# Kernel tuning notes

Hardware: AMD Instinct MI355X
Metric: run time of the kernel (lower is better)

The kernel has to match this reference:

```python
import jax, jax.numpy as jnp
from jax import lax
import numpy as np


def setup_inputs() -> dict:
    key = jax.random.key(0)
    k1, k2 = jax.random.split(key)
    x = jax.random.normal(k1, (16, 512, 512, 3), dtype=jnp.float32)
    # raw filter; module draws N(mean=10, scale=1) then normalizes to sum 1
    filt = jax.random.normal(k2, (9, 9, 1, 1), dtype=jnp.float32)
    return {"x": x, "filt": filt}


def _conv_same(a, f):
    # NHWC input, HWIO filter, SAME padding, stride 1
    return lax.conv_general_dilated(
        a, f, window_strides=(1, 1), padding="SAME",
        dimension_numbers=("NHWC", "HWIO", "NHWC"))


def reference(x, filt):
    # Keras: random_normal_variable(mean=10, scale=1) -> shift raw N(0,1) by 10
    f = filt + 10.0
    f = f / jnp.sum(f)                      # normalize BEFORE channel repeat
    f = jnp.tile(f, (1, 1, 3, 1))           # (9,9,3,1): sums over 3 input channels
    local_mean = _conv_same(x, f)           # (B,H,W,1), broadcasts over channels
    v = x - local_mean                      # (B,H,W,3)
    sigma = jnp.sqrt(_conv_same(v * v, f))  # (B,H,W,1)
    mean = jnp.mean(sigma, axis=(1, 2), keepdims=True)  # (B,1,1,1)
    return v / jnp.maximum(mean, sigma)
```

## Files before the change

kernel.cpp:

```cpp
#include <hip/hip_runtime.h>

#define BATCH 16
#define HH 512
#define WW 512
#define NPIX (BATCH * HH * WW)

#define RAD 4
#define OT 32
#define MT (OT + 2*RAD)
#define ST (MT + 2*RAD)

__global__ void norm_filter_kernel(const float* __restrict__ filt,
                                   float* __restrict__ f) {
    __shared__ float sh[128];
    int tid = threadIdx.x;
    float v = (tid < 81) ? (filt[tid] + 10.0f) : 0.0f;
    sh[tid] = v;
    __syncthreads();
    for (int o = 64; o > 0; o >>= 1) {
        if (tid < o) sh[tid] += sh[tid + o];
        __syncthreads();
    }
    float sum = sh[0];
    if (tid < 81) f[tid] = v / sum;
}

__global__ __launch_bounds__(256) void lcn_fused_kernel(
        const float* __restrict__ x, const float* __restrict__ f,
        float* __restrict__ m, float* __restrict__ sig,
        float* __restrict__ partial) {
    __shared__ float s48[ST][ST];
    __shared__ float q48[ST][ST];
    __shared__ float t40[MT][MT];
    __shared__ float wsum[4];

    const int tid = threadIdx.x;
    const int b = blockIdx.z;
    const int h0 = blockIdx.y * OT;
    const int w0 = blockIdx.x * OT;
    const float* xb = x + (size_t)b * HH * WW * 3;

#pragma unroll
    for (int k = 0; k < 9; k++) {
        const int i = tid + k * 256;
        const int r = i / ST, c = i - r * ST;
        const int gh = h0 - 2 * RAD + r, gw = w0 - 2 * RAD + c;
        float sv = 0.0f, qv = 0.0f;
        if (gh >= 0 && gh < HH && gw >= 0 && gw < WW) {
            const float* xp = xb + ((size_t)gh * WW + gw) * 3;
            float a0 = xp[0], a1 = xp[1], a2 = xp[2];
            sv = a0 + a1 + a2;
            qv = a0 * a0 + a1 * a1 + a2 * a2;
        }
        s48[r][c] = sv;
        q48[r][c] = qv;
    }
    __syncthreads();

    for (int item = tid; item < MT * (MT / 4); item += 256) {
        const int cg = item % (MT / 4);
        const int row = item / (MT / 4);
        const int c0 = 4 * cg;

        float acc0 = 0.f, acc1 = 0.f, acc2 = 0.f, acc3 = 0.f;
#pragma unroll
        for (int dh = 0; dh < 9; dh++) {
            const float4 va = *(const float4*)&s48[row + dh][c0];
            const float4 vb = *(const float4*)&s48[row + dh][c0 + 4];
            const float4 vc = *(const float4*)&s48[row + dh][c0 + 8];
            const float v[12] = {va.x, va.y, va.z, va.w,
                                 vb.x, vb.y, vb.z, vb.w,
                                 vc.x, vc.y, vc.z, vc.w};
#pragma unroll
            for (int j = 0; j < 9; j++) {
                const float fv = f[dh * 9 + j];
                acc0 += v[j] * fv;
                acc1 += v[j + 1] * fv;
                acc2 += v[j + 2] * fv;
                acc3 += v[j + 3] * fv;
            }
        }

        const float4 sc = *(const float4*)&s48[row + 4][c0 + 4];
        const float4 qc = *(const float4*)&q48[row + 4][c0 + 4];
        const int gh = h0 - RAD + row;
        const bool ghin = (gh >= 0 && gh < HH);
        const int gw0 = w0 - RAD + c0;
        float4 tv;
        tv.x = (ghin && gw0 + 0 >= 0 && gw0 + 0 < WW)
                   ? qc.x - 2.0f * acc0 * sc.x + 3.0f * acc0 * acc0 : 0.0f;
        tv.y = (ghin && gw0 + 1 >= 0 && gw0 + 1 < WW)
                   ? qc.y - 2.0f * acc1 * sc.y + 3.0f * acc1 * acc1 : 0.0f;
        tv.z = (ghin && gw0 + 2 >= 0 && gw0 + 2 < WW)
                   ? qc.z - 2.0f * acc2 * sc.z + 3.0f * acc2 * acc2 : 0.0f;
        tv.w = (ghin && gw0 + 3 >= 0 && gw0 + 3 < WW)
                   ? qc.w - 2.0f * acc3 * sc.w + 3.0f * acc3 * acc3 : 0.0f;
        *(float4*)&t40[row][c0] = tv;

        if (row >= RAD && row < RAD + OT && cg >= 1 && cg <= 8) {
            float4 mv4 = {acc0, acc1, acc2, acc3};
            *(float4*)&m[((size_t)b * HH + gh) * WW + (w0 + 4 * (cg - 1))] = mv4;
        }
    }
    __syncthreads();

    float psum = 0.0f;
    {
        const int cg = tid % (OT / 4);
        const int row = tid / (OT / 4);
        const int c0 = 4 * cg;

        float acc0 = 0.f, acc1 = 0.f, acc2 = 0.f, acc3 = 0.f;
#pragma unroll
        for (int dh = 0; dh < 9; dh++) {
            const float4 va = *(const float4*)&t40[row + dh][c0];
            const float4 vb = *(const float4*)&t40[row + dh][c0 + 4];
            const float4 vc = *(const float4*)&t40[row + dh][c0 + 8];
            const float v[12] = {va.x, va.y, va.z, va.w,
                                 vb.x, vb.y, vb.z, vb.w,
                                 vc.x, vc.y, vc.z, vc.w};
#pragma unroll
            for (int j = 0; j < 9; j++) {
                const float fv = f[dh * 9 + j];
                acc0 += v[j] * fv;
                acc1 += v[j + 1] * fv;
                acc2 += v[j + 2] * fv;
                acc3 += v[j + 3] * fv;
            }
        }
        float4 sg;
        sg.x = sqrtf(fmaxf(acc0, 0.0f));
        sg.y = sqrtf(fmaxf(acc1, 0.0f));
        sg.z = sqrtf(fmaxf(acc2, 0.0f));
        sg.w = sqrtf(fmaxf(acc3, 0.0f));
        *(float4*)&sig[((size_t)b * HH + (h0 + row)) * WW + (w0 + c0)] = sg;
        psum = sg.x + sg.y + sg.z + sg.w;
    }

#pragma unroll
    for (int o = 32; o > 0; o >>= 1) psum += __shfl_down(psum, o);
    if ((tid & 63) == 0) wsum[tid >> 6] = psum;
    __syncthreads();
    if (tid == 0)
        partial[b * 256 + blockIdx.y * 16 + blockIdx.x] =
            wsum[0] + wsum[1] + wsum[2] + wsum[3];
}

__global__ __launch_bounds__(256) void reduce_bsum_kernel(
        const float* __restrict__ partial, float* __restrict__ bsum) {
    __shared__ float wsum[4];
    const int b = blockIdx.x, tid = threadIdx.x;
    float v = partial[b * 256 + tid];
#pragma unroll
    for (int o = 32; o > 0; o >>= 1) v += __shfl_down(v, o);
    if ((tid & 63) == 0) wsum[tid >> 6] = v;
    __syncthreads();
    if (tid == 0) bsum[b] = wsum[0] + wsum[1] + wsum[2] + wsum[3];
}

__global__ __launch_bounds__(256) void final_kernel(
        const float* __restrict__ x, const float* __restrict__ m,
        const float* __restrict__ sig, const float* __restrict__ bsum,
        float* __restrict__ out) {
    const int i = blockIdx.x * 256 + threadIdx.x;
    const int b = i >> 16;
    const float mean = bsum[b] * (1.0f / (HH * WW));

    float4 mv = ((const float4*)m)[i];
    float4 sv = ((const float4*)sig)[i];
    const float4* xp = (const float4*)x + (size_t)i * 3;
    float4 a = xp[0], bb = xp[1], cc = xp[2];

    float r0 = __builtin_amdgcn_rcpf(fmaxf(mean, sv.x));
    float r1 = __builtin_amdgcn_rcpf(fmaxf(mean, sv.y));
    float r2 = __builtin_amdgcn_rcpf(fmaxf(mean, sv.z));
    float r3 = __builtin_amdgcn_rcpf(fmaxf(mean, sv.w));

    float4 o0, o1, o2;
    o0.x = (a.x - mv.x) * r0;
    o0.y = (a.y - mv.x) * r0;
    o0.z = (a.z - mv.x) * r0;
    o0.w = (a.w - mv.y) * r1;
    o1.x = (bb.x - mv.y) * r1;
    o1.y = (bb.y - mv.y) * r1;
    o1.z = (bb.z - mv.z) * r2;
    o1.w = (bb.w - mv.z) * r2;
    o2.x = (cc.x - mv.z) * r2;
    o2.y = (cc.y - mv.w) * r3;
    o2.z = (cc.z - mv.w) * r3;
    o2.w = (cc.w - mv.w) * r3;

    float4* op = (float4*)out + (size_t)i * 3;
    op[0] = o0;
    op[1] = o1;
    op[2] = o2;
}

extern "C" void kernel_launch(void* const* d_in, const int* in_sizes, int n_in,
                              void* d_out, int out_size, void* d_ws, size_t ws_size,
                              hipStream_t stream) {
    const float* x = (const float*)d_in[0];
    const float* filt = (const float*)d_in[1];
    float* out = (float*)d_out;

    char* ws = (char*)d_ws;
    float* f = (float*)ws;
    float* bsum = (float*)(ws + 512);
    float* partial = (float*)(ws + 1024);
    float* m = (float*)(ws + 32768);
    float* sig = m + NPIX;

    norm_filter_kernel<<<1, 128, 0, stream>>>(filt, f);

    dim3 cgrid(WW / OT, HH / OT, BATCH);
    lcn_fused_kernel<<<cgrid, 256, 0, stream>>>(x, f, m, sig, partial);
    reduce_bsum_kernel<<<BATCH, 256, 0, stream>>>(partial, bsum);
    final_kernel<<<NPIX / 4 / 256, 256, 0, stream>>>(x, m, sig, bsum, out);
}
```

Measured before the change: 180.1 us.

## Split fused LCN conv into separate mean and sigma conv kernels

The single fused kernel computed the first convolution over an enlarged halo (40x40 outputs from a 48x48 tile) so the second convolution could run in the same block. It is now split into two kernels: one computes the local mean and the squared deviation t per pixel over only the 32x32 output tile, and the other convolves t from global memory to get sigma and per-block partial sums. This removes the redundant halo recomputation and cuts shared-memory use per block. In exchange it adds a full-size intermediate t that must be written and read back through global memory, plus one more kernel launch.

```diff
diff --git a/kernel.cpp b/kernel.cpp
--- a/kernel.cpp
+++ b/kernel.cpp
@@ -5,10 +5,9 @@
 #define WW 512
 #define NPIX (BATCH * HH * WW)
 
+#define OT 32
 #define RAD 4
-#define OT 32
-#define MT (OT + 2*RAD)
-#define ST (MT + 2*RAD)
+#define LT (OT + 2 * RAD)
 
 __global__ void norm_filter_kernel(const float* __restrict__ filt,
                                    float* __restrict__ f) {
@@ -25,14 +24,11 @@
     if (tid < 81) f[tid] = v / sum;
 }
 
-__global__ __launch_bounds__(256) void lcn_fused_kernel(
+
+__global__ __launch_bounds__(256) void conv_mean_kernel(
         const float* __restrict__ x, const float* __restrict__ f,
-        float* __restrict__ m, float* __restrict__ sig,
-        float* __restrict__ partial) {
-    __shared__ float s48[ST][ST];
-    __shared__ float q48[ST][ST];
-    __shared__ float t40[MT][MT];
-    __shared__ float wsum[4];
+        float* __restrict__ m, float* __restrict__ t) {
+    __shared__ float tile[LT][LT];
 
     const int tid = threadIdx.x;
     const int b = blockIdx.z;
@@ -40,103 +36,121 @@
     const int w0 = blockIdx.x * OT;
     const float* xb = x + (size_t)b * HH * WW * 3;
 
-#pragma unroll
-    for (int k = 0; k < 9; k++) {
-        const int i = tid + k * 256;
-        const int r = i / ST, c = i - r * ST;
-        const int gh = h0 - 2 * RAD + r, gw = w0 - 2 * RAD + c;
-        float sv = 0.0f, qv = 0.0f;
+    for (int i = tid; i < LT * LT; i += 256) {
+        const int r = i / LT, c = i - r * LT;
+        const int gh = h0 - RAD + r, gw = w0 - RAD + c;
+        float v = 0.0f;
         if (gh >= 0 && gh < HH && gw >= 0 && gw < WW) {
             const float* xp = xb + ((size_t)gh * WW + gw) * 3;
-            float a0 = xp[0], a1 = xp[1], a2 = xp[2];
-            sv = a0 + a1 + a2;
-            qv = a0 * a0 + a1 * a1 + a2 * a2;
+            v = xp[0] + xp[1] + xp[2];
         }
-        s48[r][c] = sv;
-        q48[r][c] = qv;
-    }
-    __syncthreads();
-
-    for (int item = tid; item < MT * (MT / 4); item += 256) {
-        const int cg = item % (MT / 4);
-        const int row = item / (MT / 4);
-        const int c0 = 4 * cg;
-
-        float acc0 = 0.f, acc1 = 0.f, acc2 = 0.f, acc3 = 0.f;
-#pragma unroll
-        for (int dh = 0; dh < 9; dh++) {
-            const float4 va = *(const float4*)&s48[row + dh][c0];
-            const float4 vb = *(const float4*)&s48[row + dh][c0 + 4];
-            const float4 vc = *(const float4*)&s48[row + dh][c0 + 8];
-            const float v[12] = {va.x, va.y, va.z, va.w,
-                                 vb.x, vb.y, vb.z, vb.w,
-                                 vc.x, vc.y, vc.z, vc.w};
-#pragma unroll
-            for (int j = 0; j < 9; j++) {
-                const float fv = f[dh * 9 + j];
-                acc0 += v[j] * fv;
-                acc1 += v[j + 1] * fv;
-                acc2 += v[j + 2] * fv;
-                acc3 += v[j + 3] * fv;
-            }
+        tile[r][c] = v;
+    }
+    __syncthreads();
+
+    const int cg = tid & 7;
+    const int row = tid >> 3;
+    const int c0 = 4 * cg;
+
+    float2 a01 = {0.f, 0.f}, a23 = {0.f, 0.f};
+#pragma unroll
+    for (int dh = 0; dh < 9; dh++) {
+        const float4 va = *(const float4*)&tile[row + dh][c0];
+        const float4 vb = *(const float4*)&tile[row + dh][c0 + 4];
+        const float4 vc = *(const float4*)&tile[row + dh][c0 + 8];
+        const float v[12] = {va.x, va.y, va.z, va.w,
+                             vb.x, vb.y, vb.z, vb.w,
+                             vc.x, vc.y, vc.z, vc.w};
+#pragma unroll
+        for (int j = 0; j < 9; j++) {
+            const float fv = f[dh * 9 + j];
+            a01.x += v[j] * fv;
+            a01.y += v[j + 1] * fv;
+            a23.x += v[j + 2] * fv;
+            a23.y += v[j + 3] * fv;
         }
-
-        const float4 sc = *(const float4*)&s48[row + 4][c0 + 4];
-        const float4 qc = *(const float4*)&q48[row + 4][c0 + 4];
-        const int gh = h0 - RAD + row;
-        const bool ghin = (gh >= 0 && gh < HH);
-        const int gw0 = w0 - RAD + c0;
-        float4 tv;
-        tv.x = (ghin && gw0 + 0 >= 0 && gw0 + 0 < WW)
-                   ? qc.x - 2.0f * acc0 * sc.x + 3.0f * acc0 * acc0 : 0.0f;
-        tv.y = (ghin && gw0 + 1 >= 0 && gw0 + 1 < WW)
-                   ? qc.y - 2.0f * acc1 * sc.y + 3.0f * acc1 * acc1 : 0.0f;
-        tv.z = (ghin && gw0 + 2 >= 0 && gw0 + 2 < WW)
-                   ? qc.z - 2.0f * acc2 * sc.z + 3.0f * acc2 * acc2 : 0.0f;
-        tv.w = (ghin && gw0 + 3 >= 0 && gw0 + 3 < WW)
-                   ? qc.w - 2.0f * acc3 * sc.w + 3.0f * acc3 * acc3 : 0.0f;
-        *(float4*)&t40[row][c0] = tv;
-
-        if (row >= RAD && row < RAD + OT && cg >= 1 && cg <= 8) {
-            float4 mv4 = {acc0, acc1, acc2, acc3};
-            *(float4*)&m[((size_t)b * HH + gh) * WW + (w0 + 4 * (cg - 1))] = mv4;
+    }
+
+    const int gh = h0 + row;
+    const int gw0 = w0 + c0;
+    const size_t cbase = ((size_t)gh * WW + gw0) * 3;
+    const float4 xa = *(const float4*)&xb[cbase];
+    const float4 xc = *(const float4*)&xb[cbase + 4];
+    const float4 xe = *(const float4*)&xb[cbase + 8];
+
+    float4 tv;
+    {
+        float d0 = xa.x - a01.x, d1 = xa.y - a01.x, d2 = xa.z - a01.x;
+        tv.x = d0 * d0 + d1 * d1 + d2 * d2;
+        d0 = xa.w - a01.y; d1 = xc.x - a01.y; d2 = xc.y - a01.y;
+        tv.y = d0 * d0 + d1 * d1 + d2 * d2;
+        d0 = xc.z - a23.x; d1 = xc.w - a23.x; d2 = xe.x - a23.x;
+        tv.z = d0 * d0 + d1 * d1 + d2 * d2;
+        d0 = xe.y - a23.y; d1 = xe.z - a23.y; d2 = xe.w - a23.y;
+        tv.w = d0 * d0 + d1 * d1 + d2 * d2;
+    }
+
+    const size_t idx = ((size_t)b * HH + gh) * WW + gw0;
+    float4 mv = {a01.x, a01.y, a23.x, a23.y};
+    *(float4*)&m[idx] = mv;
+    *(float4*)&t[idx] = tv;
+}
+
+__global__ __launch_bounds__(256) void conv_sigma_kernel(
+        const float* __restrict__ t, const float* __restrict__ f,
+        float* __restrict__ sig, float* __restrict__ partial) {
+    __shared__ float tile[LT][LT];
+    __shared__ float wsum[4];
+
+    const int tid = threadIdx.x;
+    const int b = blockIdx.z;
+    const int h0 = blockIdx.y * OT;
+    const int w0 = blockIdx.x * OT;
+    const float* tb = t + (size_t)b * HH * WW;
+
+    for (int i = tid; i < LT * LT; i += 256) {
+        const int r = i / LT, c = i - r * LT;
+        const int gh = h0 - RAD + r, gw = w0 - RAD + c;
+        float v = 0.0f;
+        if (gh >= 0 && gh < HH && gw >= 0 && gw < WW)
+            v = tb[(size_t)gh * WW + gw];
+        tile[r][c] = v;
+    }
+    __syncthreads();
+
+    const int cg = tid & 7;
+    const int row = tid >> 3;
+    const int c0 = 4 * cg;
+
+    float2 a01 = {0.f, 0.f}, a23 = {0.f, 0.f};
+#pragma unroll
+    for (int dh = 0; dh < 9; dh++) {
+        const float4 va = *(const float4*)&tile[row + dh][c0];
+        const float4 vb = *(const float4*)&tile[row + dh][c0 + 4];
+        const float4 vc = *(const float4*)&tile[row + dh][c0 + 8];
+        const float v[12] = {va.x, va.y, va.z, va.w,
+                             vb.x, vb.y, vb.z, vb.w,
+                             vc.x, vc.y, vc.z, vc.w};
+#pragma unroll
+        for (int j = 0; j < 9; j++) {
+            const float fv = f[dh * 9 + j];
+            a01.x += v[j] * fv;
+            a01.y += v[j + 1] * fv;
+            a23.x += v[j + 2] * fv;
+            a23.y += v[j + 3] * fv;
         }
     }
-    __syncthreads();
-
-    float psum = 0.0f;
-    {
-        const int cg = tid % (OT / 4);
-        const int row = tid / (OT / 4);
-        const int c0 = 4 * cg;
-
-        float acc0 = 0.f, acc1 = 0.f, acc2 = 0.f, acc3 = 0.f;
-#pragma unroll
-        for (int dh = 0; dh < 9; dh++) {
-            const float4 va = *(const float4*)&t40[row + dh][c0];
-            const float4 vb = *(const float4*)&t40[row + dh][c0 + 4];
-            const float4 vc = *(const float4*)&t40[row + dh][c0 + 8];
-            const float v[12] = {va.x, va.y, va.z, va.w,
-                                 vb.x, vb.y, vb.z, vb.w,
-                                 vc.x, vc.y, vc.z, vc.w};
-#pragma unroll
-            for (int j = 0; j < 9; j++) {
-                const float fv = f[dh * 9 + j];
-                acc0 += v[j] * fv;
-                acc1 += v[j + 1] * fv;
-                acc2 += v[j + 2] * fv;
-                acc3 += v[j + 3] * fv;
-            }
-        }
-        float4 sg;
-        sg.x = sqrtf(fmaxf(acc0, 0.0f));
-        sg.y = sqrtf(fmaxf(acc1, 0.0f));
-        sg.z = sqrtf(fmaxf(acc2, 0.0f));
-        sg.w = sqrtf(fmaxf(acc3, 0.0f));
-        *(float4*)&sig[((size_t)b * HH + (h0 + row)) * WW + (w0 + c0)] = sg;
-        psum = sg.x + sg.y + sg.z + sg.w;
-    }
-
+
+    float4 sg;
+    sg.x = sqrtf(fmaxf(a01.x, 0.0f));
+    sg.y = sqrtf(fmaxf(a01.y, 0.0f));
+    sg.z = sqrtf(fmaxf(a23.x, 0.0f));
+    sg.w = sqrtf(fmaxf(a23.y, 0.0f));
+
+    const int gh = h0 + row;
+    *(float4*)&sig[((size_t)b * HH + gh) * WW + (w0 + c0)] = sg;
+
+    float psum = sg.x + sg.y + sg.z + sg.w;
 #pragma unroll
     for (int o = 32; o > 0; o >>= 1) psum += __shfl_down(psum, o);
     if ((tid & 63) == 0) wsum[tid >> 6] = psum;
@@ -208,12 +222,15 @@
     float* bsum = (float*)(ws + 512);
     float* partial = (float*)(ws + 1024);
     float* m = (float*)(ws + 32768);
-    float* sig = m + NPIX;
+    float* t = m + NPIX;
+    float* sig = t + NPIX;
 
     norm_filter_kernel<<<1, 128, 0, stream>>>(filt, f);
 
     dim3 cgrid(WW / OT, HH / OT, BATCH);
-    lcn_fused_kernel<<<cgrid, 256, 0, stream>>>(x, f, m, sig, partial);
+    conv_mean_kernel<<<cgrid, 256, 0, stream>>>(x, f, m, t);
+    conv_sigma_kernel<<<cgrid, 256, 0, stream>>>(t, f, sig, partial);
     reduce_bsum_kernel<<<BATCH, 256, 0, stream>>>(partial, bsum);
+
     final_kernel<<<NPIX / 4 / 256, 256, 0, stream>>>(x, m, sig, bsum, out);
 }
```

New measurement: 163.4 us. -9.3%, faster.
